# Kernel tuning notes

Hardware: AMD Instinct MI355X
Metric: run time of the kernel (lower is better)

The kernel has to match this reference:

```python
import jax, jax.numpy as jnp
import numpy as np

N = 1_000_000      # number of observed reflections
DMETA = 32         # metadata feature dim


def setup_inputs() -> dict:
    key = jax.random.key(0)
    k1, k2, k3, k4 = jax.random.split(key, 4)
    # positive Miller indices so gcd >= 1 (avoids division by zero)
    hkl = jax.random.randint(k1, (N, 3), 1, 51, dtype=jnp.int32)
    # resolutions in [1, 3) Angstrom, dmin = 1.0 -> 1..3 harmonics typically
    dHKL = 1.0 + 2.0 * jax.random.uniform(k2, (N, 1), dtype=jnp.float32)
    # Laue wavelength band [0.8, 1.2) Angstrom
    wavelength = 0.8 + 0.4 * jax.random.uniform(k3, (N, 1), dtype=jnp.float32)
    meta = jax.random.normal(k4, (N, DMETA), dtype=jnp.float32)
    dmin = jnp.float32(1.0)  # registered buffer in the torch module
    return {"hkl": hkl, "dHKL": dHKL, "wavelength": wavelength,
            "meta": meta, "dmin": dmin}


def _expand_indices(hkl, dHKL, dmin):
    """gcd reduction, harmonic count, and the (row idx, harmonic order) compaction."""
    g = jnp.gcd(jnp.gcd(hkl[:, 0], hkl[:, 1]), hkl[:, 2])[:, None]  # [N,1]
    d0 = dHKL * g.astype(dHKL.dtype)                                 # [N,1]
    n_max = jnp.floor_divide(d0, dmin).astype(jnp.int32)[:, 0]       # [N]
    n_big = int(n_max.max())                                         # device sync (as in torch)
    harm = jnp.arange(1, n_big + 2)                                  # [H] values 1..n_max.max()+1
    mask = harm[None, :] <= n_max[:, None]                           # [N,H]
    idx, col = jnp.nonzero(mask)                                     # ragged compaction (eager)
    n_obs = col + 1                                                  # harmonic order, 1-based
    return g, d0, idx, n_obs


def reference(hkl, dHKL, wavelength, meta, dmin):
    g, d0, idx, n_obs = _expand_indices(hkl, dHKL, dmin)
    hkl_0 = hkl // g                                   # fundamental Miller indices
    wavelength_0 = wavelength * g.astype(wavelength.dtype)
    nf = n_obs[:, None].astype(d0.dtype)
    hkl_out = hkl_0[idx] * n_obs[:, None]              # [M,3]
    dHKL_out = d0[idx] / nf                            # [M,1]
    wavelength_out = wavelength_0[idx] / nf            # [M,1]
    meta_out = meta[idx]                               # [M,DMETA]
    return hkl_out, dHKL_out, wavelength_out, meta_out
```

## Files before the change

### kernel.cpp

```cpp
#include <hip/hip_runtime.h>


typedef float f32x4 __attribute__((ext_vector_type(4)));

__device__ __forceinline__ int gcd2(int a, int b) {
    while (b) { int t = a % b; a = b; b = t; }
    return a;
}
__device__ __forceinline__ int gcd3(int a, int b, int c) {
    return gcd2(gcd2(a, b), c);
}

__device__ __forceinline__ int row_nmax(const int* __restrict__ hkl,
                                        const float* __restrict__ dHKL,
                                        float dmin, int i, int* g_out) {
    int h = hkl[3 * i], k = hkl[3 * i + 1], l = hkl[3 * i + 2];
    int g = gcd3(h, k, l);
    if (g < 1) g = 1;
    *g_out = g;
    float d0 = dHKL[i] * (float)g;
    return (int)floorf(d0 / dmin);
}

__global__ void k_count(const int* __restrict__ hkl, const float* __restrict__ dHKL,
                        const float* __restrict__ dmin_p,
                        int* __restrict__ bsums, int N) {
    int i = blockIdx.x * 256 + threadIdx.x;
    int nm = 0;
    if (i < N) {
        int g;
        nm = row_nmax(hkl, dHKL, dmin_p[0], i, &g);
    }
    __shared__ int red[256];
    red[threadIdx.x] = nm;
    __syncthreads();
    for (int s = 128; s > 0; s >>= 1) {
        if (threadIdx.x < s) red[threadIdx.x] += red[threadIdx.x + s];
        __syncthreads();
    }
    if (threadIdx.x == 0) bsums[blockIdx.x] = red[0];
}

__global__ void k_expand(const int* __restrict__ hkl, const float* __restrict__ dHKL,
                         const float* __restrict__ dmin_p, const int* __restrict__ bsums,
                         int* __restrict__ pack, int N, int M) {
    int tid = threadIdx.x;
    int i = blockIdx.x * 256 + tid;
    int nm = 0, g;
    if (i < N) nm = row_nmax(hkl, dHKL, dmin_p[0], i, &g);

    __shared__ int red[256];

    int acc = 0;
    for (int j = tid; j < (int)blockIdx.x; j += 256) acc += bsums[j];
    red[tid] = acc;
    __syncthreads();
    for (int s = 128; s > 0; s >>= 1) {
        if (tid < s) red[tid] += red[tid + s];
        __syncthreads();
    }
    int bb = red[0];
    __syncthreads();

    red[tid] = nm;
    __syncthreads();
    for (int off = 1; off < 256; off <<= 1) {
        int x = (tid >= off) ? red[tid - off] : 0;
        __syncthreads();
        red[tid] += x;
        __syncthreads();
    }
    int base = bb + red[tid] - nm;

    if (i < N) {
        int p = (i << 8);
        for (int n = 1; n <= nm; n++) {
            int m = base + n - 1;
            if (m < M) pack[m] = p | n;
        }
    }
}

__global__ void k_out(const int* __restrict__ pack, const int* __restrict__ hkl,
                      const float* __restrict__ dHKL, const float* __restrict__ wl,
                      const float* __restrict__ meta, float* __restrict__ out,
                      int M, int N, int gs,
                      int total, int pad, int nbody4, int nextra) {
    if ((int)blockIdx.x < gs) {
        __shared__ float sh[768];
        int m0 = blockIdx.x * 256;
        int m = m0 + threadIdx.x;
        int mm = (m < M) ? m : (M - 1);
        int p = pack[mm];
        int row = p >> 8;
        int n = p & 255;
        if (row >= N || row < 0 || n == 0) { row = 0; n = 1; }
        int h = hkl[3 * row], k = hkl[3 * row + 1], l = hkl[3 * row + 2];
        int g = gcd3(h, k, l);
        if (g < 1) g = 1;
        float gf = (float)g;
        float nf = (float)n;
        sh[3 * threadIdx.x]     = (float)((h / g) * n);
        sh[3 * threadIdx.x + 1] = (float)((k / g) * n);
        sh[3 * threadIdx.x + 2] = (float)((l / g) * n);
        if (m < M) {
            __builtin_nontemporal_store((dHKL[row] * gf) / nf, &out[(size_t)3 * M + m]);
            __builtin_nontemporal_store((wl[row] * gf) / nf,   &out[(size_t)4 * M + m]);
        }
        __syncthreads();
        int ob = 3 * m0;
        for (int j = (int)threadIdx.x; j < 768; j += 256) {
            int idx = ob + j;
            if (idx < 3 * M) __builtin_nontemporal_store(sh[j], &out[idx]);
        }
    } else {
        float* __restrict__ out5 = out + (size_t)5 * M;
        int t = ((int)blockIdx.x - gs) * 256 + threadIdx.x;
        if (t < nbody4) {
            int p = pad + (t << 2);
            int m0 = p >> 5;
            int ra = pack[m0] >> 8;
            if (ra >= N || ra < 0) ra = 0;
            f32x4 v;
            if (pad == 0) {
                const f32x4* meta4 = (const f32x4*)meta;
                v = meta4[(ra << 3) + ((p & 31) >> 2)];
            } else {
                int m3 = (p + 3) >> 5;
                int rb = (m3 == m0) ? ra : (pack[m3] >> 8);
                if (rb >= N || rb < 0) rb = 0;
                {
                    int pj = p;     int mj = pj >> 5; int rj = (mj == m0) ? ra : rb;
                    v.x = meta[(rj << 5) + (pj & 31)];
                }
                {
                    int pj = p + 1; int mj = pj >> 5; int rj = (mj == m0) ? ra : rb;
                    v.y = meta[(rj << 5) + (pj & 31)];
                }
                {
                    int pj = p + 2; int mj = pj >> 5; int rj = (mj == m0) ? ra : rb;
                    v.z = meta[(rj << 5) + (pj & 31)];
                }
                {
                    int pj = p + 3; int mj = pj >> 5; int rj = (mj == m0) ? ra : rb;
                    v.w = meta[(rj << 5) + (pj & 31)];
                }
            }
            __builtin_nontemporal_store(v, (f32x4*)(out5 + p));
        } else {
            int e = t - nbody4;
            if (e < nextra) {
                int p = (e < pad) ? e : (pad + (nbody4 << 2) + (e - pad));
                if (p < total) {
                    int m = p >> 5;
                    int r = pack[m] >> 8;
                    if (r >= N || r < 0) r = 0;
                    __builtin_nontemporal_store(meta[(r << 5) + (p & 31)], out5 + p);
                }
            }
        }
    }
}

extern "C" void kernel_launch(void* const* d_in, const int* in_sizes, int n_in,
                              void* d_out, int out_size, void* d_ws, size_t ws_size,
                              hipStream_t stream) {
    const int*   hkl  = (const int*)d_in[0];
    const float* dHKL = (const float*)d_in[1];
    const float* wl   = (const float*)d_in[2];
    const float* meta = (const float*)d_in[3];
    const float* dmin = (const float*)d_in[4];
    float* out = (float*)d_out;

    int N = in_sizes[0] / 3;
    int M = out_size / 37;
    if (N <= 0 || M <= 0) return;
    int nb = (N + 255) / 256;

    int* bsums = (int*)d_ws;
    int* pack  = bsums + nb;

    k_count<<<nb, 256, 0, stream>>>(hkl, dHKL, dmin, bsums, N);
    k_expand<<<nb, 256, 0, stream>>>(hkl, dHKL, dmin, bsums, pack, N, M);

    int gs = (M + 255) / 256;
    int total = 32 * M;
    int base  = 5 * M;
    int pad   = (4 - (base & 3)) & 3;
    if (pad > total) pad = total;
    int body   = total - pad;
    int nbody4 = body >> 2;
    int tail   = body & 3;
    int nextra = pad + tail;
    int gm = (nbody4 + nextra + 255) / 256;
    k_out<<<gs + gm, 256, 0, stream>>>(pack, hkl, dHKL, wl, meta, out,
                                       M, N, gs, total, pad, nbody4, nextra);
}
```

Measured before the change: 520.9 us.

## Fuse expansion and output gather into one per-row scatter kernel

Replaces the pack-index buffer and the separate per-output gather kernel with a fused kernel. Each input row computes its scan offset, loads its 32-float metadata row once into registers, and writes all harmonic copies directly. This removes the pack write/read round trip, the repeated gcd recomputation and one launch. In exchange, writes become per-thread strided scatters with variable loop lengths, which may hurt coalescing and cause divergence. It also clamps n_max to 0..255.

Result: slower. 593.6 us (+14.0%).

```diff
diff --git a/kernel.cpp b/kernel.cpp
--- a/kernel.cpp
+++ b/kernel.cpp
@@ -2,6 +2,7 @@
 
 
 typedef float f32x4 __attribute__((ext_vector_type(4)));
+typedef float f32x2 __attribute__((ext_vector_type(2)));
 
 __device__ __forceinline__ int gcd2(int a, int b) {
     while (b) { int t = a % b; a = b; b = t; }
@@ -19,7 +20,10 @@
     if (g < 1) g = 1;
     *g_out = g;
     float d0 = dHKL[i] * (float)g;
-    return (int)floorf(d0 / dmin);
+    int nm = (int)floorf(d0 / dmin);
+    if (nm < 0) nm = 0;
+    if (nm > 255) nm = 255;
+    return nm;
 }
 
 __global__ void k_count(const int* __restrict__ hkl, const float* __restrict__ dHKL,
@@ -41,12 +45,13 @@
     if (threadIdx.x == 0) bsums[blockIdx.x] = red[0];
 }
 
-__global__ void k_expand(const int* __restrict__ hkl, const float* __restrict__ dHKL,
-                         const float* __restrict__ dmin_p, const int* __restrict__ bsums,
-                         int* __restrict__ pack, int N, int M) {
+__global__ void k_fused(const int* __restrict__ hkl, const float* __restrict__ dHKL,
+                        const float* __restrict__ wl, const float* __restrict__ meta,
+                        const float* __restrict__ dmin_p, const int* __restrict__ bsums,
+                        float* __restrict__ out, int N, int M) {
     int tid = threadIdx.x;
     int i = blockIdx.x * 256 + tid;
-    int nm = 0, g;
+    int nm = 0, g = 1;
     if (i < N) nm = row_nmax(hkl, dHKL, dmin_p[0], i, &g);
 
     __shared__ int red[256];
@@ -72,91 +77,53 @@
     }
     int base = bb + red[tid] - nm;
 
-    if (i < N) {
-        int p = (i << 8);
-        for (int n = 1; n <= nm; n++) {
-            int m = base + n - 1;
-            if (m < M) pack[m] = p | n;
-        }
-    }
-}
+    if (i >= N || nm <= 0) return;
 
-__global__ void k_out(const int* __restrict__ pack, const int* __restrict__ hkl,
-                      const float* __restrict__ dHKL, const float* __restrict__ wl,
-                      const float* __restrict__ meta, float* __restrict__ out,
-                      int M, int N, int gs,
-                      int total, int pad, int nbody4, int nextra) {
-    if ((int)blockIdx.x < gs) {
-        __shared__ float sh[768];
-        int m0 = blockIdx.x * 256;
-        int m = m0 + threadIdx.x;
-        int mm = (m < M) ? m : (M - 1);
-        int p = pack[mm];
-        int row = p >> 8;
-        int n = p & 255;
-        if (row >= N || row < 0 || n == 0) { row = 0; n = 1; }
-        int h = hkl[3 * row], k = hkl[3 * row + 1], l = hkl[3 * row + 2];
-        int g = gcd3(h, k, l);
-        if (g < 1) g = 1;
-        float gf = (float)g;
+    int h = hkl[3 * i], k = hkl[3 * i + 1], l = hkl[3 * i + 2];
+    int h0 = h / g, k0 = k / g, l0 = l / g;
+    float gf = (float)g;
+    float d0 = dHKL[i] * gf;
+    float w0 = wl[i] * gf;
+
+    const f32x4* __restrict__ mrow = (const f32x4*)(meta + ((size_t)i << 5));
+    f32x4 r[8];
+#pragma unroll
+    for (int j = 0; j < 8; j++) r[j] = __builtin_nontemporal_load(mrow + j);
+
+    float* __restrict__ out3 = out + (size_t)3 * M;
+    float* __restrict__ out4 = out + (size_t)4 * M;
+    float* __restrict__ out5 = out + (size_t)5 * M;
+    int phi = (int)((5u * (unsigned)M) & 3u);
+
+    for (int n = 1; n <= nm; n++) {
+        int m = base + n - 1;
+        if ((unsigned)m >= (unsigned)M) break;
         float nf = (float)n;
-        sh[3 * threadIdx.x]     = (float)((h / g) * n);
-        sh[3 * threadIdx.x + 1] = (float)((k / g) * n);
-        sh[3 * threadIdx.x + 2] = (float)((l / g) * n);
-        if (m < M) {
-            __builtin_nontemporal_store((dHKL[row] * gf) / nf, &out[(size_t)3 * M + m]);
-            __builtin_nontemporal_store((wl[row] * gf) / nf,   &out[(size_t)4 * M + m]);
-        }
-        __syncthreads();
-        int ob = 3 * m0;
-        for (int j = (int)threadIdx.x; j < 768; j += 256) {
-            int idx = ob + j;
-            if (idx < 3 * M) __builtin_nontemporal_store(sh[j], &out[idx]);
-        }
-    } else {
-        float* __restrict__ out5 = out + (size_t)5 * M;
-        int t = ((int)blockIdx.x - gs) * 256 + threadIdx.x;
-        if (t < nbody4) {
-            int p = pad + (t << 2);
-            int m0 = p >> 5;
-            int ra = pack[m0] >> 8;
-            if (ra >= N || ra < 0) ra = 0;
-            f32x4 v;
-            if (pad == 0) {
-                const f32x4* meta4 = (const f32x4*)meta;
-                v = meta4[(ra << 3) + ((p & 31) >> 2)];
-            } else {
-                int m3 = (p + 3) >> 5;
-                int rb = (m3 == m0) ? ra : (pack[m3] >> 8);
-                if (rb >= N || rb < 0) rb = 0;
-                {
-                    int pj = p;     int mj = pj >> 5; int rj = (mj == m0) ? ra : rb;
-                    v.x = meta[(rj << 5) + (pj & 31)];
-                }
-                {
-                    int pj = p + 1; int mj = pj >> 5; int rj = (mj == m0) ? ra : rb;
-                    v.y = meta[(rj << 5) + (pj & 31)];
-                }
-                {
-                    int pj = p + 2; int mj = pj >> 5; int rj = (mj == m0) ? ra : rb;
-                    v.z = meta[(rj << 5) + (pj & 31)];
-                }
-                {
-                    int pj = p + 3; int mj = pj >> 5; int rj = (mj == m0) ? ra : rb;
-                    v.w = meta[(rj << 5) + (pj & 31)];
-                }
+        out[3 * m + 0] = (float)(h0 * n);
+        out[3 * m + 1] = (float)(k0 * n);
+        out[3 * m + 2] = (float)(l0 * n);
+        out3[m] = d0 / nf;
+        out4[m] = w0 / nf;
+        float* __restrict__ d = out5 + ((size_t)m << 5);
+        if (phi == 0) {
+            f32x4* __restrict__ d4 = (f32x4*)d;
+#pragma unroll
+            for (int j = 0; j < 8; j++) __builtin_nontemporal_store(r[j], d4 + j);
+        } else if (phi == 2) {
+#pragma unroll
+            for (int j = 0; j < 8; j++) {
+                f32x2 a = {r[j].x, r[j].y};
+                f32x2 b = {r[j].z, r[j].w};
+                __builtin_nontemporal_store(a, (f32x2*)(d + 4 * j));
+                __builtin_nontemporal_store(b, (f32x2*)(d + 4 * j + 2));
             }
-            __builtin_nontemporal_store(v, (f32x4*)(out5 + p));
         } else {
-            int e = t - nbody4;
-            if (e < nextra) {
-                int p = (e < pad) ? e : (pad + (nbody4 << 2) + (e - pad));
-                if (p < total) {
-                    int m = p >> 5;
-                    int r = pack[m] >> 8;
-                    if (r >= N || r < 0) r = 0;
-                    __builtin_nontemporal_store(meta[(r << 5) + (p & 31)], out5 + p);
-                }
+#pragma unroll
+            for (int j = 0; j < 8; j++) {
+                d[4 * j + 0] = r[j].x;
+                d[4 * j + 1] = r[j].y;
+                d[4 * j + 2] = r[j].z;
+                d[4 * j + 3] = r[j].w;
             }
         }
     }
@@ -178,21 +145,7 @@
     int nb = (N + 255) / 256;
 
     int* bsums = (int*)d_ws;
-    int* pack  = bsums + nb;
 
     k_count<<<nb, 256, 0, stream>>>(hkl, dHKL, dmin, bsums, N);
-    k_expand<<<nb, 256, 0, stream>>>(hkl, dHKL, dmin, bsums, pack, N, M);
-
-    int gs = (M + 255) / 256;
-    int total = 32 * M;
-    int base  = 5 * M;
-    int pad   = (4 - (base & 3)) & 3;
-    if (pad > total) pad = total;
-    int body   = total - pad;
-    int nbody4 = body >> 2;
-    int tail   = body & 3;
-    int nextra = pad + tail;
-    int gm = (nbody4 + nextra + 255) / 256;
-    k_out<<<gs + gm, 256, 0, stream>>>(pack, hkl, dHKL, wl, meta, out,
-                                       M, N, gs, total, pad, nbody4, nextra);
+    k_fused<<<nb, 256, 0, stream>>>(hkl, dHKL, wl, meta, dmin, bsums, out, N, M);
 }
```
